# Optimization experiments

Hardware: AMD Instinct MI355X
Metric: run time of the kernel (lower is better)

## Reference

```python
import jax, jax.numpy as jnp
import numpy as np

SIZE = 256  # output image is SIZE x SIZE


def lookup_table(size):
    # matches torch.meshgrid(indexing='ij') + stack + rot90
    lin = jnp.linspace(-1.0, 1.0, size)
    xx, yy = jnp.meshgrid(lin, lin, indexing='ij')
    t = jnp.stack([xx, yy], axis=-1)
    return jnp.rot90(t, 1, axes=(0, 1))  # [S,S,2]


def area2d(a, b, c):
    return (b[..., 0] - a[..., 0]) * (c[..., 1] - a[..., 1]) - (b[..., 1] - a[..., 1]) * (c[..., 0] - a[..., 0])


def face_normals(tris):
    n = jnp.cross(tris[:, 1] - tris[:, 0], tris[:, 2] - tris[:, 0])
    # NB: faithful to source: normalize by GLOBAL Frobenius norm (not per-face)
    return n / jnp.linalg.norm(n)


def vertex_normals(vertices, f):
    fn = face_normals(vertices[f])
    vn = jnp.zeros_like(vertices)
    vn = vn.at[f[:, 0]].add(fn).at[f[:, 1]].add(fn).at[f[:, 2]].add(fn)
    return vn / jnp.linalg.norm(vn)


def bilinear_sample(img, gx, gy):
    # torch.grid_sampler_2d, mode=bilinear, padding=zeros, align_corners=False
    # img: [C,H,W]; gx -> width axis, gy -> height axis, both in [-1,1]
    C, H, W = img.shape
    x = ((gx + 1.0) * W - 1.0) * 0.5
    y = ((gy + 1.0) * H - 1.0) * 0.5
    x0 = jnp.floor(x)
    y0 = jnp.floor(y)
    x1 = x0 + 1.0
    y1 = y0 + 1.0
    wx1 = x - x0
    wx0 = 1.0 - wx1
    wy1 = y - y0
    wy0 = 1.0 - wy1

    def gather(ix, iy):
        valid = (ix >= 0) & (ix <= W - 1) & (iy >= 0) & (iy <= H - 1)
        ixc = jnp.clip(ix, 0, W - 1).astype(jnp.int32)
        iyc = jnp.clip(iy, 0, H - 1).astype(jnp.int32)
        return img[:, iyc, ixc] * valid  # [C,...]

    return (gather(x0, y0) * (wx0 * wy0) + gather(x1, y0) * (wx1 * wy0)
            + gather(x0, y1) * (wx0 * wy1) + gather(x1, y1) * (wx1 * wy1))


def setup_inputs() -> dict:
    key = jax.random.key(0)
    k1, k2, k3, k4, k5, k6 = jax.random.split(key, 6)
    V, F, M = 1024, 256, 1024
    xy = jax.random.uniform(k1, (V, 2), minval=-1.0, maxval=1.0, dtype=jnp.float32)
    z = jax.random.uniform(k2, (V, 1), minval=0.5, maxval=1.5, dtype=jnp.float32)
    vertices = jnp.concatenate([xy, z], axis=1)
    faces = jax.random.randint(k3, (F, 3), 0, V, dtype=jnp.int64)
    uv = jax.random.uniform(k4, (M, 2), dtype=jnp.float32)
    uvfaces = jax.random.randint(k5, (F, 3), 0, M, dtype=jnp.int64)
    uvmap = jax.random.uniform(k6, (3, 256, 256), dtype=jnp.float32)
    return {"vertices": vertices, "faces": faces, "uv": uv, "uvfaces": uvfaces, "uvmap": uvmap}


def reference(vertices, faces, uv, uvfaces, uvmap):
    size = SIZE
    pts = lookup_table(size)                       # [S,S,2]
    uvn = uv * 2.0 - 1.0                            # init: uv*2-1
    tris = vertices[faces]                          # [F,3,3]
    z_inv = 1.0 / tris[:, :, 2:3]                   # [F,3,1]
    vn = vertex_normals(vertices, faces)[faces] * z_inv
    uvs = uvn[uvfaces] * z_inv
    tri9 = jnp.concatenate([tris, uvs, vn, z_inv], axis=2)  # [F,3,9]
    cullmask = face_normals(tris)[:, 2] > 0         # backface cull, eye=(0,0,1)

    t2 = tris[:, :, :2]
    A = area2d(t2[:, 0], t2[:, 1], t2[:, 2])        # [F] signed double-area
    valid_tri = cullmask & (A >= 1e-9)              # raster skips A < 1e-9
    Asafe = jnp.where(jnp.abs(A) < 1e-9, 1.0, A)

    px = pts[..., 0][None]                          # [1,S,S]
    py = pts[..., 1][None]

    def edge(a, c):
        # area2d(a, p, c) evaluated on the pixel grid: linear in p
        ax, ay = a[:, 0, None, None], a[:, 1, None, None]
        cx, cy = c[:, 0, None, None], c[:, 1, None, None]
        return (px - ax) * (cy - ay) - (py - ay) * (cx - ax)

    pAB = edge(t2[:, 1], t2[:, 0])                  # [F,S,S]
    pCB = edge(t2[:, 2], t2[:, 1])
    pCA = edge(t2[:, 0], t2[:, 2])
    cover = (pAB > 0) & (pCB > 0) & (pCA > 0) & valid_tri[:, None, None]

    w1 = pCB / Asafe[:, None, None]
    w2 = pCA / Asafe[:, None, None]
    w3 = 1.0 - w1 - w2
    zinv_p = (w1 * tri9[:, 0, 8, None, None] + w2 * tri9[:, 1, 8, None, None]
              + w3 * tri9[:, 2, 8, None, None])     # interpolated 1/z, [F,S,S]
    zinit = vertices[:, 2].min()                    # initial z-buffer value
    ptsZ = 1.0 / jnp.where(cover, zinv_p, 1.0)      # perspective-correct depth
    score = jnp.where(cover & (ptsZ >= zinit), ptsZ, -jnp.inf)
    # sequential loop with `ptsZ >= zbuffer` converges to the max-depth winner
    winner = jnp.argmax(score, axis=0)              # [S,S]
    hit = jnp.isfinite(jnp.max(score, axis=0))      # [S,S]

    take = lambda arr: jnp.take_along_axis(arr, winner[None], axis=0)[0]
    W1, W2, W3 = take(w1), take(w2), take(w3)       # [S,S]
    tri_w = tri9[winner]                            # [S,S,3,9]
    pts9 = (W1[..., None] * tri_w[..., 0, :] + W2[..., None] * tri_w[..., 1, :]
            + W3[..., None] * tri_w[..., 2, :])     # [S,S,9]
    Zw = 1.0 / jnp.where(hit, pts9[..., 8], 1.0)
    attrs = pts9[..., :8] * Zw[..., None]           # perspective-corrected attrs
    rgb = bilinear_sample(uvmap, attrs[..., 3], attrs[..., 4])  # [3,S,S]
    hitf = hit.astype(rgb.dtype)
    result = jnp.concatenate([rgb * hitf[None], hitf[None]], axis=0)  # [4,S,S]
    return result
```

## Files before the change

### kernel.cpp

```cpp
#include <hip/hip_runtime.h>
#include <math.h>
#include <limits.h>

#define SIZE   256
#define NFACES 256
#define NVERTS 1024
#define NSPLIT 8


__global__ __launch_bounds__(256) void prep_kernel(
    const float* __restrict__ vertices,
    const int*   __restrict__ faces,
    const float* __restrict__ uv,
    const int*   __restrict__ uvfaces,
    float* __restrict__ ws)
{
#pragma clang fp contract(off)
    __shared__ float wred[4];
    __shared__ int   wcnt[4];
    const int t    = threadIdx.x;
    const int lane = t & 63;
    const int wv   = t >> 6;

    {
        float m =    vertices[3*t         + 2];
        m = fminf(m, vertices[3*(t + 256) + 2]);
        m = fminf(m, vertices[3*(t + 512) + 2]);
        m = fminf(m, vertices[3*(t + 768) + 2]);
        for (int off = 32; off > 0; off >>= 1) m = fminf(m, __shfl_down(m, off));
        if (lane == 0) wred[wv] = m;
    }

    const int i0 = faces[3*t+0], i1 = faces[3*t+1], i2 = faces[3*t+2];
    const float ax = vertices[3*i0+0], ay = vertices[3*i0+1], az = vertices[3*i0+2];
    const float bx = vertices[3*i1+0], by = vertices[3*i1+1], bz = vertices[3*i1+2];
    const float cx = vertices[3*i2+0], cy = vertices[3*i2+1], cz = vertices[3*i2+2];
    const float A  = (bx-ax)*(cy-ay) - (by-ay)*(cx-ax);
    const bool keep = (A >= 1e-9f);
    const unsigned long long bmask = __ballot(keep);
    const int rank = __popcll(bmask & ((1ull << lane) - 1ull));
    if (lane == 0) wcnt[wv] = (int)__popcll(bmask);
    __syncthreads();

    if (t == 0) {
        ((int*)ws)[0] = wcnt[0] + wcnt[1] + wcnt[2] + wcnt[3];
        ws[1] = fminf(fminf(wred[0], wred[1]), fminf(wred[2], wred[3]));
    }
    if (keep) {
        int base = 0;
        #pragma unroll
        for (int w = 0; w < 4; ++w) if (w < wv) base += wcnt[w];
        const int slot = base + rank;
        const float z0i = 1.0f/az, z1i = 1.0f/bz, z2i = 1.0f/cz;
        const int j0 = uvfaces[3*t+0], j1 = uvfaces[3*t+1], j2 = uvfaces[3*t+2];
        const float2 u0 = *reinterpret_cast<const float2*>(&uv[2*j0]);
        const float2 u1 = *reinterpret_cast<const float2*>(&uv[2*j1]);
        const float2 u2 = *reinterpret_cast<const float2*>(&uv[2*j2]);
        float4* rec = reinterpret_cast<float4*>(ws + 4) + slot*5;
        rec[0] = make_float4(fminf(fminf(ax,bx),cx), fmaxf(fmaxf(ax,bx),cx),
                             fminf(fminf(ay,by),cy), fmaxf(fmaxf(ay,by),cy));
        rec[1] = make_float4(ax, ay, bx, by);
        rec[2] = make_float4(cx, cy, z0i, z1i);
        rec[3] = make_float4(z2i, A,
                             (u0.x*2.0f - 1.0f) * z0i,
                             (u0.y*2.0f - 1.0f) * z0i);
        rec[4] = make_float4((u1.x*2.0f - 1.0f) * z1i,
                             (u1.y*2.0f - 1.0f) * z1i,
                             (u2.x*2.0f - 1.0f) * z2i,
                             (u2.y*2.0f - 1.0f) * z2i);
    }
}

__global__ __launch_bounds__(1024) void render_kernel(
    const float* __restrict__ uvmap,
    const float* __restrict__ ws,
    float* __restrict__ out)
{
#pragma clang fp contract(off)
    __shared__ float sh_best[NSPLIT][128];
    __shared__ int   sh_slot[NSPLIT][128];

    const int t    = threadIdx.x;
    const int half = blockIdx.x;
    const int row  = blockIdx.y;
    const int col  = (t & 127) + 128 * half;
    const int grp  = t >> 7;

    const float px = (float)(-1.0 + (double)col         * (2.0/255.0));
    const float py = (float)(-1.0 + (double)(255 - row) * (2.0/255.0));

    const int   nv    = ((const int*)ws)[0];
    const float zinit = ws[1];
    const float4* __restrict__ recs = reinterpret_cast<const float4*>(ws + 4);

    const int   c0   = ((t >> 6) & 1) * 64 + 128 * half;
    const float pxlo = (float)(-1.0 + (double)c0        * (2.0/255.0));
    const float pxhi = (float)(-1.0 + (double)(c0 + 63) * (2.0/255.0));

    const int cs = (nv + NSPLIT - 1) / NSPLIT;
    int f0 = grp * cs; if (f0 > nv) f0 = nv;
    int f1 = f0 + cs;  if (f1 > nv) f1 = nv;

    float best  = -INFINITY;
    int   wslot = 0;
    for (int i = f0; i < f1; ++i) {
        const float4 bb = recs[i*5];
        if (bb.y + 1e-4f < pxlo || bb.x - 1e-4f > pxhi ||
            py <= bb.z - 1e-4f || py >= bb.w + 1e-4f) continue;
        const float4 r1 = recs[i*5+1];
        const float4 r2 = recs[i*5+2];
        const float4 r3 = recs[i*5+3];
        const float pAB = (px - r1.z)*(r1.y - r1.w) - (py - r1.w)*(r1.x - r1.z);
        const float pCB = (px - r2.x)*(r1.w - r2.y) - (py - r2.y)*(r1.z - r2.x);
        const float pCA = (px - r1.x)*(r2.y - r1.y) - (py - r1.y)*(r2.x - r1.x);
        if (pAB > 0.0f && pCB > 0.0f && pCA > 0.0f) {
            const float w1 = pCB / r3.y;
            const float w2 = pCA / r3.y;
            const float w3 = (1.0f - w1) - w2;
            const float zp = (w1*r2.z + w2*r2.w) + w3*r3.x;
            const float z  = 1.0f / zp;
            if (z >= zinit && z > best) { best = z; wslot = i; }
        }
    }
    sh_best[grp][t & 127] = best;
    sh_slot[grp][t & 127] = wslot;
    __syncthreads();

    if (t < 128) {
        best = -INFINITY; wslot = 0;
        #pragma unroll
        for (int g = 0; g < NSPLIT; ++g) {
            const float z = sh_best[g][t];
            const int   s = sh_slot[g][t];
            if (z > best || (z == best && s < wslot)) { best = z; wslot = s; }
        }

        const bool  hit = (best > -INFINITY);
        const float hf  = hit ? 1.0f : 0.0f;
        float r0v = 0.0f, r1v = 0.0f, r2v = 0.0f;

        if (hit) {
            const float4 r1 = recs[wslot*5+1];
            const float4 r2 = recs[wslot*5+2];
            const float4 r3 = recs[wslot*5+3];
            const float4 r4 = recs[wslot*5+4];
            const float pCB = (px - r2.x)*(r1.w - r2.y) - (py - r2.y)*(r1.z - r2.x);
            const float pCA = (px - r1.x)*(r2.y - r1.y) - (py - r1.y)*(r2.x - r1.x);
            const float w1 = pCB / r3.y;
            const float w2 = pCA / r3.y;
            const float w3 = (1.0f - w1) - w2;
            const float p3 = (w1*r3.z + w2*r4.x) + w3*r4.z;
            const float p4 = (w1*r3.w + w2*r4.y) + w3*r4.w;
            const float p8 = (w1*r2.z + w2*r2.w) + w3*r3.x;
            const float Zw = 1.0f / p8;
            const float gx = p3 * Zw;
            const float gy = p4 * Zw;

            const float x = ((gx + 1.0f)*256.0f - 1.0f)*0.5f;
            const float y = ((gy + 1.0f)*256.0f - 1.0f)*0.5f;
            const float x0f = floorf(x), y0f = floorf(y);
            const float x1f = x0f + 1.0f, y1f = y0f + 1.0f;
            const float wx1 = x - x0f, wx0 = 1.0f - wx1;
            const float wy1 = y - y0f, wy0 = 1.0f - wy1;
            const float w00 = wx0*wy0, w10 = wx1*wy0, w01 = wx0*wy1, w11 = wx1*wy1;

            {
                const bool v = (x0f >= 0.0f) && (x0f <= 255.0f) && (y0f >= 0.0f) && (y0f <= 255.0f);
                const int ix = (int)fminf(fmaxf(x0f, 0.0f), 255.0f);
                const int iy = (int)fminf(fmaxf(y0f, 0.0f), 255.0f);
                const int o  = iy*256 + ix;
                const float g0 = v ? uvmap[o]          : 0.0f;
                const float g1 = v ? uvmap[65536 + o]  : 0.0f;
                const float g2 = v ? uvmap[131072 + o] : 0.0f;
                r0v = r0v + g0*w00; r1v = r1v + g1*w00; r2v = r2v + g2*w00;
            }
            {
                const bool v = (x1f >= 0.0f) && (x1f <= 255.0f) && (y0f >= 0.0f) && (y0f <= 255.0f);
                const int ix = (int)fminf(fmaxf(x1f, 0.0f), 255.0f);
                const int iy = (int)fminf(fmaxf(y0f, 0.0f), 255.0f);
                const int o  = iy*256 + ix;
                const float g0 = v ? uvmap[o]          : 0.0f;
                const float g1 = v ? uvmap[65536 + o]  : 0.0f;
                const float g2 = v ? uvmap[131072 + o] : 0.0f;
                r0v = r0v + g0*w10; r1v = r1v + g1*w10; r2v = r2v + g2*w10;
            }
            {
                const bool v = (x0f >= 0.0f) && (x0f <= 255.0f) && (y1f >= 0.0f) && (y1f <= 255.0f);
                const int ix = (int)fminf(fmaxf(x0f, 0.0f), 255.0f);
                const int iy = (int)fminf(fmaxf(y1f, 0.0f), 255.0f);
                const int o  = iy*256 + ix;
                const float g0 = v ? uvmap[o]          : 0.0f;
                const float g1 = v ? uvmap[65536 + o]  : 0.0f;
                const float g2 = v ? uvmap[131072 + o] : 0.0f;
                r0v = r0v + g0*w01; r1v = r1v + g1*w01; r2v = r2v + g2*w01;
            }
            {
                const bool v = (x1f >= 0.0f) && (x1f <= 255.0f) && (y1f >= 0.0f) && (y1f <= 255.0f);
                const int ix = (int)fminf(fmaxf(x1f, 0.0f), 255.0f);
                const int iy = (int)fminf(fmaxf(y1f, 0.0f), 255.0f);
                const int o  = iy*256 + ix;
                const float g0 = v ? uvmap[o]          : 0.0f;
                const float g1 = v ? uvmap[65536 + o]  : 0.0f;
                const float g2 = v ? uvmap[131072 + o] : 0.0f;
                r0v = r0v + g0*w11; r1v = r1v + g1*w11; r2v = r2v + g2*w11;
            }
        }

        const int pix = row*256 + col;
        out[           pix] = r0v*hf;
        out[ 65536 +   pix] = r1v*hf;
        out[131072 +   pix] = r2v*hf;
        out[196608 +   pix] = hf;
    }
}

extern "C" void kernel_launch(void* const* d_in, const int* in_sizes, int n_in,
                              void* d_out, int out_size, void* d_ws, size_t ws_size,
                              hipStream_t stream) {
    const float* vertices = (const float*)d_in[0];
    const int*   faces    = (const int*)  d_in[1];
    const float* uv       = (const float*)d_in[2];
    const int*   uvfaces  = (const int*)  d_in[3];
    const float* uvmap    = (const float*)d_in[4];
    float*       out      = (float*)d_out;
    float*       ws       = (float*)d_ws;

    prep_kernel<<<1, 256, 0, stream>>>(vertices, faces, uv, uvfaces, ws);
    dim3 grid(2, SIZE);
    render_kernel<<<grid, 1024, 0, stream>>>(uvmap, ws, out);
}
```

Baseline: 79.72 us.

## Fuse face preprocessing into render kernel with per-block shared-memory face records

Removes the separate single-block prep kernel and has every render block load vertices, faces and uv into LDS and build its own face records there. Degenerate faces are no longer compacted; instead they get an empty bounding box so the per-pixel loop skips them over a fixed range. This removes one kernel launch, the serialization between the two kernels and the global-memory round trip for face records. In exchange, all 512 blocks redo the same preprocessing and use a large LDS footprint (about 50KB), which may limit occupancy.

```diff
diff --git a/kernel.cpp b/kernel.cpp
--- a/kernel.cpp
+++ b/kernel.cpp
@@ -7,80 +7,27 @@
 #define NVERTS 1024
 #define NSPLIT 8
 
-
-__global__ __launch_bounds__(256) void prep_kernel(
+__global__ __launch_bounds__(1024) void render_kernel(
     const float* __restrict__ vertices,
     const int*   __restrict__ faces,
     const float* __restrict__ uv,
     const int*   __restrict__ uvfaces,
-    float* __restrict__ ws)
+    const float* __restrict__ uvmap,
+    float* __restrict__ out)
 {
 #pragma clang fp contract(off)
-    __shared__ float wred[4];
-    __shared__ int   wcnt[4];
+    __shared__ float  sv[NVERTS*3];
+    __shared__ int    sf[NFACES*3];
+    __shared__ int    suvf[NFACES*3];
+    __shared__ float  suv[NVERTS*2];
+    __shared__ float4 fdl[NFACES*5];
+    __shared__ float  sh_best[NSPLIT][128];
+    __shared__ int    sh_slot[NSPLIT][128];
+    __shared__ float  wred[16];
+
     const int t    = threadIdx.x;
     const int lane = t & 63;
     const int wv   = t >> 6;
-
-    {
-        float m =    vertices[3*t         + 2];
-        m = fminf(m, vertices[3*(t + 256) + 2]);
-        m = fminf(m, vertices[3*(t + 512) + 2]);
-        m = fminf(m, vertices[3*(t + 768) + 2]);
-        for (int off = 32; off > 0; off >>= 1) m = fminf(m, __shfl_down(m, off));
-        if (lane == 0) wred[wv] = m;
-    }
-
-    const int i0 = faces[3*t+0], i1 = faces[3*t+1], i2 = faces[3*t+2];
-    const float ax = vertices[3*i0+0], ay = vertices[3*i0+1], az = vertices[3*i0+2];
-    const float bx = vertices[3*i1+0], by = vertices[3*i1+1], bz = vertices[3*i1+2];
-    const float cx = vertices[3*i2+0], cy = vertices[3*i2+1], cz = vertices[3*i2+2];
-    const float A  = (bx-ax)*(cy-ay) - (by-ay)*(cx-ax);
-    const bool keep = (A >= 1e-9f);
-    const unsigned long long bmask = __ballot(keep);
-    const int rank = __popcll(bmask & ((1ull << lane) - 1ull));
-    if (lane == 0) wcnt[wv] = (int)__popcll(bmask);
-    __syncthreads();
-
-    if (t == 0) {
-        ((int*)ws)[0] = wcnt[0] + wcnt[1] + wcnt[2] + wcnt[3];
-        ws[1] = fminf(fminf(wred[0], wred[1]), fminf(wred[2], wred[3]));
-    }
-    if (keep) {
-        int base = 0;
-        #pragma unroll
-        for (int w = 0; w < 4; ++w) if (w < wv) base += wcnt[w];
-        const int slot = base + rank;
-        const float z0i = 1.0f/az, z1i = 1.0f/bz, z2i = 1.0f/cz;
-        const int j0 = uvfaces[3*t+0], j1 = uvfaces[3*t+1], j2 = uvfaces[3*t+2];
-        const float2 u0 = *reinterpret_cast<const float2*>(&uv[2*j0]);
-        const float2 u1 = *reinterpret_cast<const float2*>(&uv[2*j1]);
-        const float2 u2 = *reinterpret_cast<const float2*>(&uv[2*j2]);
-        float4* rec = reinterpret_cast<float4*>(ws + 4) + slot*5;
-        rec[0] = make_float4(fminf(fminf(ax,bx),cx), fmaxf(fmaxf(ax,bx),cx),
-                             fminf(fminf(ay,by),cy), fmaxf(fmaxf(ay,by),cy));
-        rec[1] = make_float4(ax, ay, bx, by);
-        rec[2] = make_float4(cx, cy, z0i, z1i);
-        rec[3] = make_float4(z2i, A,
-                             (u0.x*2.0f - 1.0f) * z0i,
-                             (u0.y*2.0f - 1.0f) * z0i);
-        rec[4] = make_float4((u1.x*2.0f - 1.0f) * z1i,
-                             (u1.y*2.0f - 1.0f) * z1i,
-                             (u2.x*2.0f - 1.0f) * z2i,
-                             (u2.y*2.0f - 1.0f) * z2i);
-    }
-}
-
-__global__ __launch_bounds__(1024) void render_kernel(
-    const float* __restrict__ uvmap,
-    const float* __restrict__ ws,
-    float* __restrict__ out)
-{
-#pragma clang fp contract(off)
-    __shared__ float sh_best[NSPLIT][128];
-    __shared__ int   sh_slot[NSPLIT][128];
-
-    const int t    = threadIdx.x;
     const int half = blockIdx.x;
     const int row  = blockIdx.y;
     const int col  = (t & 127) + 128 * half;
@@ -89,27 +36,72 @@
     const float px = (float)(-1.0 + (double)col         * (2.0/255.0));
     const float py = (float)(-1.0 + (double)(255 - row) * (2.0/255.0));
 
-    const int   nv    = ((const int*)ws)[0];
-    const float zinit = ws[1];
-    const float4* __restrict__ recs = reinterpret_cast<const float4*>(ws + 4);
+    {
+        float m = vertices[3*t + 2];
+        for (int off = 32; off > 0; off >>= 1) m = fminf(m, __shfl_down(m, off));
+        if (lane == 0) wred[wv] = m;
+    }
+
+    sv[t]        = vertices[t];
+    sv[t + 1024] = vertices[t + 1024];
+    sv[t + 2048] = vertices[t + 2048];
+    suv[t]        = uv[t];
+    suv[t + 1024] = uv[t + 1024];
+    if (t < NFACES*3) {
+        sf[t]   = faces[t];
+        suvf[t] = uvfaces[t];
+    }
+    __syncthreads();
+
+    if (t < NFACES) {
+        const int i0 = sf[3*t+0], i1 = sf[3*t+1], i2 = sf[3*t+2];
+        const float ax = sv[3*i0+0], ay = sv[3*i0+1], az = sv[3*i0+2];
+        const float bx = sv[3*i1+0], by = sv[3*i1+1], bz = sv[3*i1+2];
+        const float cx = sv[3*i2+0], cy = sv[3*i2+1], cz = sv[3*i2+2];
+        const float A  = (bx-ax)*(cy-ay) - (by-ay)*(cx-ax);
+        float4* rec = &fdl[t*5];
+        if (A >= 1e-9f) {
+            const float z0i = 1.0f/az, z1i = 1.0f/bz, z2i = 1.0f/cz;
+            const int j0 = suvf[3*t+0], j1 = suvf[3*t+1], j2 = suvf[3*t+2];
+            rec[0] = make_float4(fminf(fminf(ax,bx),cx), fmaxf(fmaxf(ax,bx),cx),
+                                 fminf(fminf(ay,by),cy), fmaxf(fmaxf(ay,by),cy));
+            rec[1] = make_float4(ax, ay, bx, by);
+            rec[2] = make_float4(cx, cy, z0i, z1i);
+            rec[3] = make_float4(z2i, A,
+                                 (suv[2*j0+0]*2.0f - 1.0f) * z0i,
+                                 (suv[2*j0+1]*2.0f - 1.0f) * z0i);
+            rec[4] = make_float4((suv[2*j1+0]*2.0f - 1.0f) * z1i,
+                                 (suv[2*j1+1]*2.0f - 1.0f) * z1i,
+                                 (suv[2*j2+0]*2.0f - 1.0f) * z2i,
+                                 (suv[2*j2+1]*2.0f - 1.0f) * z2i);
+        } else {
+            rec[0] = make_float4(INFINITY, -INFINITY, INFINITY, -INFINITY);
+        }
+    }
+    __syncthreads();
+
+    float zinit;
+    {
+        float mm = wred[0];
+        #pragma unroll
+        for (int i = 1; i < 16; ++i) mm = fminf(mm, wred[i]);
+        zinit = mm;
+    }
 
     const int   c0   = ((t >> 6) & 1) * 64 + 128 * half;
     const float pxlo = (float)(-1.0 + (double)c0        * (2.0/255.0));
     const float pxhi = (float)(-1.0 + (double)(c0 + 63) * (2.0/255.0));
 
-    const int cs = (nv + NSPLIT - 1) / NSPLIT;
-    int f0 = grp * cs; if (f0 > nv) f0 = nv;
-    int f1 = f0 + cs;  if (f1 > nv) f1 = nv;
-
     float best  = -INFINITY;
     int   wslot = 0;
-    for (int i = f0; i < f1; ++i) {
-        const float4 bb = recs[i*5];
+    const int f0 = grp * (NFACES / NSPLIT);
+    for (int i = f0; i < f0 + NFACES/NSPLIT; ++i) {
+        const float4 bb = fdl[i*5];
         if (bb.y + 1e-4f < pxlo || bb.x - 1e-4f > pxhi ||
             py <= bb.z - 1e-4f || py >= bb.w + 1e-4f) continue;
-        const float4 r1 = recs[i*5+1];
-        const float4 r2 = recs[i*5+2];
-        const float4 r3 = recs[i*5+3];
+        const float4 r1 = fdl[i*5+1];
+        const float4 r2 = fdl[i*5+2];
+        const float4 r3 = fdl[i*5+3];
         const float pAB = (px - r1.z)*(r1.y - r1.w) - (py - r1.w)*(r1.x - r1.z);
         const float pCB = (px - r2.x)*(r1.w - r2.y) - (py - r2.y)*(r1.z - r2.x);
         const float pCA = (px - r1.x)*(r2.y - r1.y) - (py - r1.y)*(r2.x - r1.x);
@@ -140,10 +132,10 @@
         float r0v = 0.0f, r1v = 0.0f, r2v = 0.0f;
 
         if (hit) {
-            const float4 r1 = recs[wslot*5+1];
-            const float4 r2 = recs[wslot*5+2];
-            const float4 r3 = recs[wslot*5+3];
-            const float4 r4 = recs[wslot*5+4];
+            const float4 r1 = fdl[wslot*5+1];
+            const float4 r2 = fdl[wslot*5+2];
+            const float4 r3 = fdl[wslot*5+3];
+            const float4 r4 = fdl[wslot*5+4];
             const float pCB = (px - r2.x)*(r1.w - r2.y) - (py - r2.y)*(r1.z - r2.x);
             const float pCA = (px - r1.x)*(r2.y - r1.y) - (py - r1.y)*(r2.x - r1.x);
             const float w1 = pCB / r3.y;
@@ -223,9 +215,7 @@
     const int*   uvfaces  = (const int*)  d_in[3];
     const float* uvmap    = (const float*)d_in[4];
     float*       out      = (float*)d_out;
-    float*       ws       = (float*)d_ws;
-
-    prep_kernel<<<1, 256, 0, stream>>>(vertices, faces, uv, uvfaces, ws);
+
     dim3 grid(2, SIZE);
-    render_kernel<<<grid, 1024, 0, stream>>>(uvmap, ws, out);
+    render_kernel<<<grid, 1024, 0, stream>>>(vertices, faces, uv, uvfaces, uvmap, out);
 }
```

Measured after the change: 75.26 us. -5.6%, faster.
